# Performance work log

Hardware: AMD Instinct MI355X
Metric: run time of the kernel (lower is better)

Reference implementation:

```python
import jax, jax.numpy as jnp
import numpy as np

B, C, N, D, F = 2048, 64, 64, 64, 128  # batch, cin_hidden, num_features, embed_dim, feature_maps


def setup_inputs() -> dict:
    key = jax.random.key(0)
    k1, k2, k3 = jax.random.split(key, 3)
    xj = jax.random.normal(k1, (B, C, D), dtype=jnp.float32)
    x0 = jax.random.normal(k2, (B, N, D), dtype=jnp.float32)
    # xavier_uniform_ on (F, C, N): fan_in = C*N? torch treats dim1 as fan_in-ish;
    # exact init distribution is irrelevant for correctness testing, use scaled uniform.
    limit = float(np.sqrt(6.0 / (C + N)))
    W = jax.random.uniform(k3, (F, C, N), dtype=jnp.float32, minval=-limit, maxval=limit)
    return {"xj": xj, "x0": x0, "W": W}


def reference(xj, x0, W):
    # Original: hadamard[b,c,n,d] = x0[b,n,d]*xj[b,c,d];
    # out[b,f,c,d] = sum_n hadamard * W[f,c,n]; cin_out = sum_c out; cin_p_out = sum_d cin_out.
    # Fused: cin_out[b,f,d] = sum_{c,n} W[f,c,n] * xj[b,c,d] * x0[b,n,d]
    cin_out = jnp.einsum('bcd,bnd,fcn->bfd', xj, x0, W)  # (B, F, D)
    cin_p_out = jnp.sum(cin_out, axis=-1)  # (B, F)
    return (cin_out, cin_p_out)
```

## Files before the change

### kernel.cpp

```cpp
#include <hip/hip_runtime.h>


typedef _Float16 f16;
typedef __attribute__((ext_vector_type(8))) _Float16 half8;
typedef __attribute__((ext_vector_type(2))) _Float16 half2v;
typedef __attribute__((ext_vector_type(16))) float f32x16;
typedef __attribute__((ext_vector_type(4))) float f32x4;

#define MFMA(a, b, c) __builtin_amdgcn_mfma_f32_32x32x16_f16(a, b, c, 0, 0, 0)

union H8 { half8 v; half2v h[4]; };

__device__ __forceinline__ half8 scale8(half8 a, half2v hh) {
  H8 in, out;
  in.v = a;
  out.h[0] = in.h[0] * hh;
  out.h[1] = in.h[1] * hh;
  out.h[2] = in.h[2] * hh;
  out.h[3] = in.h[3] * hh;
  return out.v;
}

__global__ __launch_bounds__(256) void wscat_kernel(const float* __restrict__ W,
                                                    f16* __restrict__ Wb) {
  const int tid = blockIdx.x * 256 + threadIdx.x;
  const int c = tid >> 10, s = tid & 1023;
  const int gk = s >> 6, ln = s & 63;
  const int g = gk >> 2, kk = gk & 3, hi = ln >> 5, lr = ln & 31;
  const int f = g * 32 + lr, n0 = kk * 16 + hi * 8;
  const float* src = W + (size_t)f * 4096 + c * 64 + n0;
  const float4 a = *(const float4*)src;
  const float4 b = *(const float4*)(src + 4);
  half8 r;
  r[0] = (f16)a.x; r[1] = (f16)a.y; r[2] = (f16)a.z; r[3] = (f16)a.w;
  r[4] = (f16)b.x; r[5] = (f16)b.y; r[6] = (f16)b.z; r[7] = (f16)b.w;
  *(half8*)(Wb + (size_t)c * 8192 + s * 8) = r;
}

__global__ __launch_bounds__(256, 2) void cin_kernel(
    const float* __restrict__ xj, const float* __restrict__ x0,
    const f16* __restrict__ Wb, float* __restrict__ out,
    float* __restrict__ pout) {
  __shared__ f16 x0T[2 * 4096];
  __shared__ f16 xjL[2 * 4096];

  const int t = threadIdx.x;
  const int wid = t >> 6, lane = t & 63;
  const int b0 = blockIdx.x * 2;

#pragma unroll
  for (int bb = 0; bb < 2; ++bb) {
    const float* s0 = x0 + (size_t)(b0 + bb) * 4096;
    const float* sj = xj + (size_t)(b0 + bb) * 4096;
    {
      const int n = lane, d0 = wid * 16;
      const int chb = n >> 3, sub = n & 7;
#pragma unroll
      for (int q = 0; q < 4; ++q) {
        const float4 v = *(const float4*)(s0 + n * 64 + d0 + q * 4);
#pragma unroll
        for (int j = 0; j < 4; ++j) {
          const int d = d0 + q * 4 + j;
          x0T[bb * 4096 + d * 64 + ((chb ^ (d & 7)) << 3) + sub] =
              (f16)(((const float*)&v)[j]);
        }
      }
    }
#pragma unroll
    for (int p = 0; p < 4; ++p) {
      const int e = p * 1024 + t * 4;
      const float4 v = *(const float4*)(sj + e);
      f16* dst = &xjL[bb * 4096 + e];
      dst[0] = (f16)v.x; dst[1] = (f16)v.y; dst[2] = (f16)v.z; dst[3] = (f16)v.w;
    }
  }
  __syncthreads();

  const int wg = wid;
  const int lr = lane & 31, hi = lane >> 5;

  half8 af[4][4];
#pragma unroll
  for (int mf = 0; mf < 4; ++mf) {
    const int bb = mf >> 1;
    const int d = (mf & 1) * 32 + lr;
#pragma unroll
    for (int kk = 0; kk < 4; ++kk)
      af[mf][kk] = *(const half8*)&x0T[bb * 4096 + d * 64 +
                                       (((kk * 2 + hi) ^ (d & 7)) << 3)];
  }

  f32x16 acc[4] = {};

  const half8* wp = (const half8*)Wb + wg * 256 + lane;
  const f16* xjA = &xjL[lr];
  const f16* xjB = &xjL[lr] + 64;

  half8 wA0 = wp[0],    wA1 = wp[64],        wA2 = wp[128],        wA3 = wp[192];
  half8 wB0 = wp[1024], wB1 = wp[1024 + 64], wB2 = wp[1024 + 128], wB3 = wp[1024 + 192];
  f16 xA0 = xjA[0], xA1 = xjA[32], xA2 = xjA[4096], xA3 = xjA[4096 + 32];
  f16 xB0 = xjB[0], xB1 = xjB[32], xB2 = xjB[4096], xB3 = xjB[4096 + 32];

  const half8* wpA = wp + 2048;
  const half8* wpB = wp + 3072;
  const f16* xjpA = xjA + 128;
  const f16* xjpB = xjB + 128;

#pragma unroll 1
  for (int cc = 0; cc < 32; ++cc) {
    {
      const half2v h0 = {xA0, xA0}, h1 = {xA1, xA1}, h2 = {xA2, xA2}, h3 = {xA3, xA3};
      __builtin_amdgcn_s_setprio(1);
#pragma unroll
      for (int kk = 0; kk < 4; ++kk) {
        const half8 w = (kk == 0) ? wA0 : (kk == 1) ? wA1 : (kk == 2) ? wA2 : wA3;
        acc[0] = MFMA(scale8(af[0][kk], h0), w, acc[0]);
        acc[1] = MFMA(scale8(af[1][kk], h1), w, acc[1]);
        acc[2] = MFMA(scale8(af[2][kk], h2), w, acc[2]);
        acc[3] = MFMA(scale8(af[3][kk], h3), w, acc[3]);
      }
      __builtin_amdgcn_s_setprio(0);
      if (cc < 31) {
        wA0 = wpA[0]; wA1 = wpA[64]; wA2 = wpA[128]; wA3 = wpA[192];
        xA0 = xjpA[0]; xA1 = xjpA[32]; xA2 = xjpA[4096]; xA3 = xjpA[4096 + 32];
        wpA += 2048; xjpA += 128;
      }
    }
    {
      const half2v h0 = {xB0, xB0}, h1 = {xB1, xB1}, h2 = {xB2, xB2}, h3 = {xB3, xB3};
      __builtin_amdgcn_s_setprio(1);
#pragma unroll
      for (int kk = 0; kk < 4; ++kk) {
        const half8 w = (kk == 0) ? wB0 : (kk == 1) ? wB1 : (kk == 2) ? wB2 : wB3;
        acc[0] = MFMA(scale8(af[0][kk], h0), w, acc[0]);
        acc[1] = MFMA(scale8(af[1][kk], h1), w, acc[1]);
        acc[2] = MFMA(scale8(af[2][kk], h2), w, acc[2]);
        acc[3] = MFMA(scale8(af[3][kk], h3), w, acc[3]);
      }
      __builtin_amdgcn_s_setprio(0);
      if (cc < 31) {
        wB0 = wpB[0]; wB1 = wpB[64]; wB2 = wpB[128]; wB3 = wpB[192];
        xB0 = xjpB[0]; xB1 = xjpB[32]; xB2 = xjpB[4096]; xB3 = xjpB[4096 + 32];
        wpB += 2048; xjpB += 128;
      }
    }
  }

  const int fcol = wg * 32 + lr;
  float ps[4];
#pragma unroll
  for (int mf = 0; mf < 4; ++mf) {
    const int b = b0 + (mf >> 1);
    float* ob = out + (size_t)b * 8192 + (size_t)fcol * 64 + (mf & 1) * 32;
    const f32x16 v = acc[mf];
    float s = 0.f;
#pragma unroll
    for (int q = 0; q < 4; ++q) {
      f32x4 vv = { v[4 * q], v[4 * q + 1], v[4 * q + 2], v[4 * q + 3] };
      *(f32x4*)(ob + q * 8 + hi * 4) = vv;
      s += vv[0] + vv[1] + vv[2] + vv[3];
    }
    ps[mf] = s;
  }
  float pA = ps[0] + ps[1];
  float pB = ps[2] + ps[3];
  pA += __shfl_xor(pA, 32, 64);
  pB += __shfl_xor(pB, 32, 64);
  if (hi == 0) {
    pout[(size_t)b0 * 128 + fcol] = pA;
    pout[(size_t)(b0 + 1) * 128 + fcol] = pB;
  }
}

extern "C" void kernel_launch(void* const* d_in, const int* in_sizes, int n_in,
                              void* d_out, int out_size, void* d_ws, size_t ws_size,
                              hipStream_t stream) {
  const float* xj = (const float*)d_in[0];
  const float* x0 = (const float*)d_in[1];
  const float* W  = (const float*)d_in[2];
  float* out  = (float*)d_out;
  float* pout = out + (size_t)2048 * 128 * 64;
  f16* Wb = (f16*)d_ws;

  wscat_kernel<<<256, 256, 0, stream>>>(W, Wb);
  cin_kernel<<<1024, 256, 0, stream>>>(xj, x0, Wb, out, pout);
}
```

Baseline: 139.7 us.

## Split block work across 8 waves, one batch per wave group

Doubles the block size to 512 threads so each wave handles a single batch element (two M-fragments) instead of both batches (four). This halves the accumulators and A-fragment registers per wave, raising occupancy and wave-level parallelism for MFMA latency hiding. The trade-off is that each W fragment loaded from global/L2 now feeds only two MFMAs per wave instead of four, doubling weight-load traffic per unit of compute. The xj staging store is also vectorized to half4.

```diff
diff --git a/kernel.cpp b/kernel.cpp
--- a/kernel.cpp
+++ b/kernel.cpp
@@ -3,6 +3,7 @@
 
 typedef _Float16 f16;
 typedef __attribute__((ext_vector_type(8))) _Float16 half8;
+typedef __attribute__((ext_vector_type(4))) _Float16 half4;
 typedef __attribute__((ext_vector_type(2))) _Float16 half2v;
 typedef __attribute__((ext_vector_type(16))) float f32x16;
 typedef __attribute__((ext_vector_type(4))) float f32x4;
@@ -37,7 +38,7 @@
   *(half8*)(Wb + (size_t)c * 8192 + s * 8) = r;
 }
 
-__global__ __launch_bounds__(256, 2) void cin_kernel(
+__global__ __launch_bounds__(512, 4) void cin_kernel(
     const float* __restrict__ xj, const float* __restrict__ x0,
     const f16* __restrict__ Wb, float* __restrict__ out,
     float* __restrict__ pout) {
@@ -45,15 +46,15 @@
   __shared__ f16 xjL[2 * 4096];
 
   const int t = threadIdx.x;
-  const int wid = t >> 6, lane = t & 63;
   const int b0 = blockIdx.x * 2;
 
-#pragma unroll
-  for (int bb = 0; bb < 2; ++bb) {
-    const float* s0 = x0 + (size_t)(b0 + bb) * 4096;
-    const float* sj = xj + (size_t)(b0 + bb) * 4096;
+  {
+    const int sel = t >> 8, th = t & 255;
+    const int wid8 = th >> 6, lane8 = th & 63;
+    const float* s0 = x0 + (size_t)(b0 + sel) * 4096;
+    const float* sj = xj + (size_t)(b0 + sel) * 4096;
     {
-      const int n = lane, d0 = wid * 16;
+      const int n = lane8, d0 = wid8 * 16;
       const int chb = n >> 3, sub = n & 7;
 #pragma unroll
       for (int q = 0; q < 4; ++q) {
@@ -61,45 +62,45 @@
 #pragma unroll
         for (int j = 0; j < 4; ++j) {
           const int d = d0 + q * 4 + j;
-          x0T[bb * 4096 + d * 64 + ((chb ^ (d & 7)) << 3) + sub] =
+          x0T[sel * 4096 + d * 64 + ((chb ^ (d & 7)) << 3) + sub] =
               (f16)(((const float*)&v)[j]);
         }
       }
     }
 #pragma unroll
     for (int p = 0; p < 4; ++p) {
-      const int e = p * 1024 + t * 4;
+      const int e = p * 1024 + th * 4;
       const float4 v = *(const float4*)(sj + e);
-      f16* dst = &xjL[bb * 4096 + e];
-      dst[0] = (f16)v.x; dst[1] = (f16)v.y; dst[2] = (f16)v.z; dst[3] = (f16)v.w;
+      half4 r; r[0] = (f16)v.x; r[1] = (f16)v.y; r[2] = (f16)v.z; r[3] = (f16)v.w;
+      *(half4*)&xjL[sel * 4096 + e] = r;
     }
   }
   __syncthreads();
 
-  const int wg = wid;
+  const int wid = t >> 6, lane = t & 63;
+  const int bb = wid >> 2, wg = wid & 3;
   const int lr = lane & 31, hi = lane >> 5;
 
-  half8 af[4][4];
+  half8 af[2][4];
 #pragma unroll
-  for (int mf = 0; mf < 4; ++mf) {
-    const int bb = mf >> 1;
-    const int d = (mf & 1) * 32 + lr;
+  for (int dh = 0; dh < 2; ++dh) {
+    const int d = dh * 32 + lr;
 #pragma unroll
     for (int kk = 0; kk < 4; ++kk)
-      af[mf][kk] = *(const half8*)&x0T[bb * 4096 + d * 64 +
+      af[dh][kk] = *(const half8*)&x0T[bb * 4096 + d * 64 +
                                        (((kk * 2 + hi) ^ (d & 7)) << 3)];
   }
 
-  f32x16 acc[4] = {};
+  f32x16 acc[2] = {};
 
   const half8* wp = (const half8*)Wb + wg * 256 + lane;
-  const f16* xjA = &xjL[lr];
-  const f16* xjB = &xjL[lr] + 64;
+  const f16* xjA = &xjL[bb * 4096 + lr];
+  const f16* xjB = xjA + 64;
 
   half8 wA0 = wp[0],    wA1 = wp[64],        wA2 = wp[128],        wA3 = wp[192];
   half8 wB0 = wp[1024], wB1 = wp[1024 + 64], wB2 = wp[1024 + 128], wB3 = wp[1024 + 192];
-  f16 xA0 = xjA[0], xA1 = xjA[32], xA2 = xjA[4096], xA3 = xjA[4096 + 32];
-  f16 xB0 = xjB[0], xB1 = xjB[32], xB2 = xjB[4096], xB3 = xjB[4096 + 32];
+  f16 xA0 = xjA[0], xA1 = xjA[32];
+  f16 xB0 = xjB[0], xB1 = xjB[32];
 
   const half8* wpA = wp + 2048;
   const half8* wpB = wp + 3072;
@@ -109,67 +110,55 @@
 #pragma unroll 1
   for (int cc = 0; cc < 32; ++cc) {
     {
-      const half2v h0 = {xA0, xA0}, h1 = {xA1, xA1}, h2 = {xA2, xA2}, h3 = {xA3, xA3};
+      const half2v h0 = {xA0, xA0}, h1 = {xA1, xA1};
       __builtin_amdgcn_s_setprio(1);
 #pragma unroll
       for (int kk = 0; kk < 4; ++kk) {
         const half8 w = (kk == 0) ? wA0 : (kk == 1) ? wA1 : (kk == 2) ? wA2 : wA3;
         acc[0] = MFMA(scale8(af[0][kk], h0), w, acc[0]);
         acc[1] = MFMA(scale8(af[1][kk], h1), w, acc[1]);
-        acc[2] = MFMA(scale8(af[2][kk], h2), w, acc[2]);
-        acc[3] = MFMA(scale8(af[3][kk], h3), w, acc[3]);
       }
       __builtin_amdgcn_s_setprio(0);
       if (cc < 31) {
         wA0 = wpA[0]; wA1 = wpA[64]; wA2 = wpA[128]; wA3 = wpA[192];
-        xA0 = xjpA[0]; xA1 = xjpA[32]; xA2 = xjpA[4096]; xA3 = xjpA[4096 + 32];
+        xA0 = xjpA[0]; xA1 = xjpA[32];
         wpA += 2048; xjpA += 128;
       }
     }
     {
-      const half2v h0 = {xB0, xB0}, h1 = {xB1, xB1}, h2 = {xB2, xB2}, h3 = {xB3, xB3};
+      const half2v h0 = {xB0, xB0}, h1 = {xB1, xB1};
       __builtin_amdgcn_s_setprio(1);
 #pragma unroll
       for (int kk = 0; kk < 4; ++kk) {
         const half8 w = (kk == 0) ? wB0 : (kk == 1) ? wB1 : (kk == 2) ? wB2 : wB3;
         acc[0] = MFMA(scale8(af[0][kk], h0), w, acc[0]);
         acc[1] = MFMA(scale8(af[1][kk], h1), w, acc[1]);
-        acc[2] = MFMA(scale8(af[2][kk], h2), w, acc[2]);
-        acc[3] = MFMA(scale8(af[3][kk], h3), w, acc[3]);
       }
       __builtin_amdgcn_s_setprio(0);
       if (cc < 31) {
         wB0 = wpB[0]; wB1 = wpB[64]; wB2 = wpB[128]; wB3 = wpB[192];
-        xB0 = xjpB[0]; xB1 = xjpB[32]; xB2 = xjpB[4096]; xB3 = xjpB[4096 + 32];
+        xB0 = xjpB[0]; xB1 = xjpB[32];
         wpB += 2048; xjpB += 128;
       }
     }
   }
 
   const int fcol = wg * 32 + lr;
-  float ps[4];
+  const int b = b0 + bb;
+  float* ob = out + (size_t)b * 8192 + (size_t)fcol * 64;
+  float psum = 0.f;
 #pragma unroll
-  for (int mf = 0; mf < 4; ++mf) {
-    const int b = b0 + (mf >> 1);
-    float* ob = out + (size_t)b * 8192 + (size_t)fcol * 64 + (mf & 1) * 32;
-    const f32x16 v = acc[mf];
-    float s = 0.f;
+  for (int dh = 0; dh < 2; ++dh) {
+    const f32x16 v = acc[dh];
 #pragma unroll
     for (int q = 0; q < 4; ++q) {
       f32x4 vv = { v[4 * q], v[4 * q + 1], v[4 * q + 2], v[4 * q + 3] };
-      *(f32x4*)(ob + q * 8 + hi * 4) = vv;
-      s += vv[0] + vv[1] + vv[2] + vv[3];
+      *(f32x4*)(ob + dh * 32 + q * 8 + hi * 4) = vv;
+      psum += vv[0] + vv[1] + vv[2] + vv[3];
     }
-    ps[mf] = s;
   }
-  float pA = ps[0] + ps[1];
-  float pB = ps[2] + ps[3];
-  pA += __shfl_xor(pA, 32, 64);
-  pB += __shfl_xor(pB, 32, 64);
-  if (hi == 0) {
-    pout[(size_t)b0 * 128 + fcol] = pA;
-    pout[(size_t)(b0 + 1) * 128 + fcol] = pB;
-  }
+  psum += __shfl_xor(psum, 32, 64);
+  if (hi == 0) pout[(size_t)b * 128 + fcol] = psum;
 }
 
 extern "C" void kernel_launch(void* const* d_in, const int* in_sizes, int n_in,
@@ -183,5 +172,5 @@
   f16* Wb = (f16*)d_ws;
 
   wscat_kernel<<<256, 256, 0, stream>>>(W, Wb);
-  cin_kernel<<<1024, 256, 0, stream>>>(xj, x0, Wb, out, pout);
+  cin_kernel<<<1024, 512, 0, stream>>>(xj, x0, Wb, out, pout);
 }
```

Result: slower. 161.2 us (+15.4%).

## Stage weight tiles through LDS with async global_load_lds triple buffering

Applied to the files above, without the earlier changes.

Replaces the per-wave direct global loads of the fp16 weight fragments with async global_load_lds copies into a three-slot LDS ring, prefetching three channels ahead with explicit vmcnt waits and barriers each phase. It also repacks xj in LDS so both batches' scalars come from one half2 load. The goal is to share each weight tile across the block and hide global latency behind the MFMA work. In exchange it adds a block-wide barrier per channel and raises LDS use to 64KB per block, which may limit occupancy.

```diff
diff --git a/kernel.cpp b/kernel.cpp
--- a/kernel.cpp
+++ b/kernel.cpp
@@ -8,6 +8,10 @@
 typedef __attribute__((ext_vector_type(4))) float f32x4;
 
 #define MFMA(a, b, c) __builtin_amdgcn_mfma_f32_32x32x16_f16(a, b, c, 0, 0, 0)
+
+#define GLOAD16(g, l) __builtin_amdgcn_global_load_lds( \
+    (const __attribute__((address_space(1))) void*)(g), \
+    (__attribute__((address_space(3))) void*)(l), 16, 0, 0)
 
 union H8 { half8 v; half2v h[4]; };
 
@@ -37,47 +41,92 @@
   *(half8*)(Wb + (size_t)c * 8192 + s * 8) = r;
 }
 
+#define X0T 16384
+#define XJ0 24576
+
+#define PHASE(CEXPR, BUF, CUR, NXT) do {                                       \
+  const int c_ = (CEXPR);                                                      \
+  { const int cs_ = (c_ + 3 <= 63) ? (c_ + 3) : 63;                            \
+    const f16* gs_ = Wb + (size_t)cs_ * 8192;                                  \
+    _Pragma("unroll")                                                          \
+    for (int p = 0; p < 4; ++p)                                                \
+      GLOAD16(gs_ + (p * 256 + t) * 8,                                         \
+              &S[BUF * 8192 + (p * 256 + (wid << 6)) * 8]); }                  \
+  { const int cn_ = (c_ + 1 <= 63) ? (c_ + 1) : 63;                            \
+    const f16* ws_ = &S[((BUF + 1) % 3) * 8192 + wg * 2048 + lane * 8];        \
+    w##NXT##0 = *(const half8*)(ws_ + 0 * 512);                                \
+    w##NXT##1 = *(const half8*)(ws_ + 1 * 512);                                \
+    w##NXT##2 = *(const half8*)(ws_ + 2 * 512);                                \
+    w##NXT##3 = *(const half8*)(ws_ + 3 * 512);                                \
+    xj##NXT##0 = *(const half2v*)&S[XJ0 + cn_ * 128 + lr * 2];                 \
+    xj##NXT##1 = *(const half2v*)&S[XJ0 + cn_ * 128 + (32 + lr) * 2]; }        \
+  { const half2v h0 = {xj##CUR##0[0], xj##CUR##0[0]};                          \
+    const half2v h1 = {xj##CUR##1[0], xj##CUR##1[0]};                          \
+    const half2v h2 = {xj##CUR##0[1], xj##CUR##0[1]};                          \
+    const half2v h3 = {xj##CUR##1[1], xj##CUR##1[1]};                          \
+    __builtin_amdgcn_s_setprio(1);                                             \
+    _Pragma("unroll")                                                          \
+    for (int kk = 0; kk < 4; ++kk) {                                           \
+      const half8 wv = (kk == 0) ? w##CUR##0 : (kk == 1) ? w##CUR##1 :         \
+                       (kk == 2) ? w##CUR##2 : w##CUR##3;                      \
+      acc[0] = MFMA(scale8(af[0][kk], h0), wv, acc[0]);                        \
+      acc[1] = MFMA(scale8(af[1][kk], h1), wv, acc[1]);                        \
+      acc[2] = MFMA(scale8(af[2][kk], h2), wv, acc[2]);                        \
+      acc[3] = MFMA(scale8(af[3][kk], h3), wv, acc[3]); }                      \
+    __builtin_amdgcn_s_setprio(0); }                                           \
+  asm volatile("s_waitcnt vmcnt(4) lgkmcnt(0)" ::: "memory");                  \
+  __builtin_amdgcn_s_barrier();                                                \
+  __builtin_amdgcn_sched_barrier(0);                                           \
+} while (0)
+
 __global__ __launch_bounds__(256, 2) void cin_kernel(
     const float* __restrict__ xj, const float* __restrict__ x0,
     const f16* __restrict__ Wb, float* __restrict__ out,
     float* __restrict__ pout) {
-  __shared__ f16 x0T[2 * 4096];
-  __shared__ f16 xjL[2 * 4096];
+  __shared__ f16 S[32768];
 
   const int t = threadIdx.x;
   const int wid = t >> 6, lane = t & 63;
   const int b0 = blockIdx.x * 2;
+  const int wg = wid;
+  const int lr = lane & 31, hi = lane >> 5;
 
 #pragma unroll
   for (int bb = 0; bb < 2; ++bb) {
     const float* s0 = x0 + (size_t)(b0 + bb) * 4096;
-    const float* sj = xj + (size_t)(b0 + bb) * 4096;
-    {
-      const int n = lane, d0 = wid * 16;
-      const int chb = n >> 3, sub = n & 7;
-#pragma unroll
-      for (int q = 0; q < 4; ++q) {
-        const float4 v = *(const float4*)(s0 + n * 64 + d0 + q * 4);
-#pragma unroll
-        for (int j = 0; j < 4; ++j) {
-          const int d = d0 + q * 4 + j;
-          x0T[bb * 4096 + d * 64 + ((chb ^ (d & 7)) << 3) + sub] =
-              (f16)(((const float*)&v)[j]);
-        }
+    const int n = lane, d0 = wid * 16;
+    const int chb = n >> 3, sub = n & 7;
+#pragma unroll
+    for (int q = 0; q < 4; ++q) {
+      const float4 v = *(const float4*)(s0 + n * 64 + d0 + q * 4);
+#pragma unroll
+      for (int j = 0; j < 4; ++j) {
+        const int d = d0 + q * 4 + j;
+        S[X0T + bb * 4096 + d * 64 + ((chb ^ (d & 7)) << 3) + sub] =
+            (f16)(((const float*)&v)[j]);
       }
     }
-#pragma unroll
-    for (int p = 0; p < 4; ++p) {
-      const int e = p * 1024 + t * 4;
-      const float4 v = *(const float4*)(sj + e);
-      f16* dst = &xjL[bb * 4096 + e];
-      dst[0] = (f16)v.x; dst[1] = (f16)v.y; dst[2] = (f16)v.z; dst[3] = (f16)v.w;
+  }
+  {
+    const int bb = t >> 7, r = t & 127, cr = r >> 1, dn = (r & 1) * 32;
+    const float* sj = xj + (size_t)(b0 + bb) * 4096 + cr * 64 + dn;
+#pragma unroll
+    for (int q = 0; q < 8; ++q) {
+      const float4 v = *(const float4*)(sj + q * 4);
+#pragma unroll
+      for (int j = 0; j < 4; ++j)
+        S[XJ0 + cr * 128 + (dn + q * 4 + j) * 2 + bb] =
+            (f16)(((const float*)&v)[j]);
     }
   }
   __syncthreads();
 
-  const int wg = wid;
-  const int lr = lane & 31, hi = lane >> 5;
+#pragma unroll
+  for (int cc = 0; cc < 2; ++cc)
+#pragma unroll
+    for (int p = 0; p < 4; ++p)
+      GLOAD16(Wb + (size_t)cc * 8192 + (p * 256 + t) * 8,
+              &S[cc * 8192 + (p * 256 + (wid << 6)) * 8]);
 
   half8 af[4][4];
 #pragma unroll
@@ -86,64 +135,63 @@
     const int d = (mf & 1) * 32 + lr;
 #pragma unroll
     for (int kk = 0; kk < 4; ++kk)
-      af[mf][kk] = *(const half8*)&x0T[bb * 4096 + d * 64 +
-                                       (((kk * 2 + hi) ^ (d & 7)) << 3)];
-  }
+      af[mf][kk] = *(const half8*)&S[X0T + bb * 4096 + d * 64 +
+                                     (((kk * 2 + hi) ^ (d & 7)) << 3)];
+  }
+  half2v xjA0 = *(const half2v*)&S[XJ0 + lr * 2];
+  half2v xjA1 = *(const half2v*)&S[XJ0 + (32 + lr) * 2];
+  half2v xjB0, xjB1;
+
+  asm volatile("s_waitcnt vmcnt(4) lgkmcnt(0)" ::: "memory");
+  __builtin_amdgcn_s_barrier();
+
+#pragma unroll
+  for (int p = 0; p < 4; ++p)
+    GLOAD16(Wb + (size_t)2 * 8192 + (p * 256 + t) * 8,
+            &S[2 * 8192 + (p * 256 + (wid << 6)) * 8]);
+
+  half8 wA0, wA1, wA2, wA3, wB0, wB1, wB2, wB3;
+  {
+    const f16* ws = &S[wg * 2048 + lane * 8];
+    wA0 = *(const half8*)(ws + 0 * 512);
+    wA1 = *(const half8*)(ws + 1 * 512);
+    wA2 = *(const half8*)(ws + 2 * 512);
+    wA3 = *(const half8*)(ws + 3 * 512);
+  }
+  asm volatile("s_waitcnt vmcnt(4) lgkmcnt(0)" ::: "memory");
+  __builtin_amdgcn_s_barrier();
+  __builtin_amdgcn_sched_barrier(0);
 
   f32x16 acc[4] = {};
 
-  const half8* wp = (const half8*)Wb + wg * 256 + lane;
-  const f16* xjA = &xjL[lr];
-  const f16* xjB = &xjL[lr] + 64;
-
-  half8 wA0 = wp[0],    wA1 = wp[64],        wA2 = wp[128],        wA3 = wp[192];
-  half8 wB0 = wp[1024], wB1 = wp[1024 + 64], wB2 = wp[1024 + 128], wB3 = wp[1024 + 192];
-  f16 xA0 = xjA[0], xA1 = xjA[32], xA2 = xjA[4096], xA3 = xjA[4096 + 32];
-  f16 xB0 = xjB[0], xB1 = xjB[32], xB2 = xjB[4096], xB3 = xjB[4096 + 32];
-
-  const half8* wpA = wp + 2048;
-  const half8* wpB = wp + 3072;
-  const f16* xjpA = xjA + 128;
-  const f16* xjpB = xjB + 128;
-
 #pragma unroll 1
-  for (int cc = 0; cc < 32; ++cc) {
-    {
-      const half2v h0 = {xA0, xA0}, h1 = {xA1, xA1}, h2 = {xA2, xA2}, h3 = {xA3, xA3};
-      __builtin_amdgcn_s_setprio(1);
-#pragma unroll
-      for (int kk = 0; kk < 4; ++kk) {
-        const half8 w = (kk == 0) ? wA0 : (kk == 1) ? wA1 : (kk == 2) ? wA2 : wA3;
-        acc[0] = MFMA(scale8(af[0][kk], h0), w, acc[0]);
-        acc[1] = MFMA(scale8(af[1][kk], h1), w, acc[1]);
-        acc[2] = MFMA(scale8(af[2][kk], h2), w, acc[2]);
-        acc[3] = MFMA(scale8(af[3][kk], h3), w, acc[3]);
-      }
-      __builtin_amdgcn_s_setprio(0);
-      if (cc < 31) {
-        wA0 = wpA[0]; wA1 = wpA[64]; wA2 = wpA[128]; wA3 = wpA[192];
-        xA0 = xjpA[0]; xA1 = xjpA[32]; xA2 = xjpA[4096]; xA3 = xjpA[4096 + 32];
-        wpA += 2048; xjpA += 128;
-      }
-    }
-    {
-      const half2v h0 = {xB0, xB0}, h1 = {xB1, xB1}, h2 = {xB2, xB2}, h3 = {xB3, xB3};
-      __builtin_amdgcn_s_setprio(1);
-#pragma unroll
-      for (int kk = 0; kk < 4; ++kk) {
-        const half8 w = (kk == 0) ? wB0 : (kk == 1) ? wB1 : (kk == 2) ? wB2 : wB3;
-        acc[0] = MFMA(scale8(af[0][kk], h0), w, acc[0]);
-        acc[1] = MFMA(scale8(af[1][kk], h1), w, acc[1]);
-        acc[2] = MFMA(scale8(af[2][kk], h2), w, acc[2]);
-        acc[3] = MFMA(scale8(af[3][kk], h3), w, acc[3]);
-      }
-      __builtin_amdgcn_s_setprio(0);
-      if (cc < 31) {
-        wB0 = wpB[0]; wB1 = wpB[64]; wB2 = wpB[128]; wB3 = wpB[192];
-        xB0 = xjpB[0]; xB1 = xjpB[32]; xB2 = xjpB[4096]; xB3 = xjpB[4096 + 32];
-        wpB += 2048; xjpB += 128;
-      }
-    }
+  for (int i = 0; i < 10; ++i) {
+    const int cb = 6 * i;
+    PHASE(cb + 0, 0, A, B);
+    PHASE(cb + 1, 1, B, A);
+    PHASE(cb + 2, 2, A, B);
+    PHASE(cb + 3, 0, B, A);
+    PHASE(cb + 4, 1, A, B);
+    PHASE(cb + 5, 2, B, A);
+  }
+  PHASE(60, 0, A, B);
+  PHASE(61, 1, B, A);
+  PHASE(62, 2, A, B);
+  {
+    const half2v h0 = {xjB0[0], xjB0[0]};
+    const half2v h1 = {xjB1[0], xjB1[0]};
+    const half2v h2 = {xjB0[1], xjB0[1]};
+    const half2v h3 = {xjB1[1], xjB1[1]};
+    __builtin_amdgcn_s_setprio(1);
+#pragma unroll
+    for (int kk = 0; kk < 4; ++kk) {
+      const half8 wv = (kk == 0) ? wB0 : (kk == 1) ? wB1 : (kk == 2) ? wB2 : wB3;
+      acc[0] = MFMA(scale8(af[0][kk], h0), wv, acc[0]);
+      acc[1] = MFMA(scale8(af[1][kk], h1), wv, acc[1]);
+      acc[2] = MFMA(scale8(af[2][kk], h2), wv, acc[2]);
+      acc[3] = MFMA(scale8(af[3][kk], h3), wv, acc[3]);
+    }
+    __builtin_amdgcn_s_setprio(0);
   }
 
   const int fcol = wg * 32 + lr;
```

Result: slower. 148.0 us (+5.9%).
